# Kernel tuning notes

Hardware: AMD Instinct MI355X
Metric: run time of the kernel (lower is better)

Reference implementation:

```python
import jax, jax.numpy as jnp
import numpy as np

B, H, W, C, E, TOP_K = 16, 64, 64, 384, 5, 2


def setup_inputs() -> dict:
    key = jax.random.key(0)
    k1, k2, k3 = jax.random.split(key, 3)
    x = jax.random.normal(k1, (B, H, W, C), dtype=jnp.float32)
    Wg = jax.random.normal(k2, (C, E), dtype=jnp.float32) * 0.02   # router
    We = jax.random.normal(k3, (E, C, C), dtype=jnp.float32) * 0.02  # expert weights
    be = jnp.zeros((E, C), dtype=jnp.float32)                       # expert biases
    return {"x": x, "Wg": Wg, "We": We, "be": be}


def reference(x, Wg, We, be):
    Bx, Hx, Wx, Cx = x.shape
    Ex = Wg.shape[1]
    t = x.reshape(-1, Cx)                      # [N, C] tokens
    N = t.shape[0]

    # --- top-k routing ---
    logits = t @ Wg                            # [N, E]
    top_vals, top_idx = jax.lax.top_k(logits, TOP_K)   # [N, 2]
    gates = jax.nn.softmax(top_vals, axis=-1)          # softmax over selected experts
    combine = jnp.zeros((N, Ex), dtype=t.dtype)
    combine = combine.at[jnp.arange(N)[:, None], top_idx].set(gates)  # [N, E] sparse combine weights

    # --- expert computation (dense over experts, combined with sparse gates) ---
    expert_out = jnp.einsum('nc,ecd->ned', t, We) + be[None]  # [N, E, C]
    y = jnp.einsum('ne,ned->nd', combine, expert_out)         # [N, C]

    # --- LeakyReLU (default slope 0.01); dropout is identity in eval mode ---
    y = jax.nn.leaky_relu(y, negative_slope=0.01)
    return y.reshape(Bx, Hx, Wx, Cx)
```

## Files before the change

kernel.cpp:

```cpp
#include <hip/hip_runtime.h>
#include <stdint.h>

#define TOKENS 65536
#define CDIM 384
#define NEXP 5
#define NPAIR 10
#define CAP 8192
#define NBLK 1024
#define WE_STRIDE (CDIM * CDIM)

typedef __attribute__((ext_vector_type(8))) short short8;
typedef __attribute__((ext_vector_type(4))) float floatx4;

__constant__ int PAIR_A[NPAIR] = {0, 0, 0, 0, 1, 1, 1, 2, 2, 3};
__constant__ int PAIR_B[NPAIR] = {1, 2, 3, 4, 2, 3, 4, 3, 4, 4};

__device__ inline unsigned short f2bf(float f) {
    union { float f; uint32_t u; } v; v.f = f;
    uint32_t r = v.u + 0x7fffu + ((v.u >> 16) & 1u);
    return (unsigned short)(r >> 16);
}

__device__ inline void load_lds16(const void* g, void* l) {
    __builtin_amdgcn_global_load_lds((const __attribute__((address_space(1))) void*)g,
                                     (__attribute__((address_space(3))) void*)l, 16, 0, 0);
}

__global__ __launch_bounds__(256) void router_kernel(const float* __restrict__ x,
                                                     const float* __restrict__ Wg,
                                                     int* __restrict__ blkcnt,
                                                     int* __restrict__ tmeta,
                                                     float2* __restrict__ tgate) {
    __shared__ __align__(16) float  xs[64 * 129];
    __shared__ __align__(16) float  wgs[CDIM * 8];
    __shared__ __align__(16) double part[4 * 64 * NEXP];
    __shared__ __align__(16) double lg[64 * NEXP];
    int t = threadIdx.x, lane = t & 63, w = t >> 6;
    int tok0 = blockIdx.x * 64;

    for (int i = t; i < CDIM * NEXP; i += 256) wgs[(i / NEXP) * 8 + (i % NEXP)] = Wg[i];

    int lrow = t >> 5, loff = (t & 31) * 4;
    double p0 = 0, p1 = 0, p2 = 0, p3 = 0, p4 = 0;
    #pragma unroll
    for (int ch = 0; ch < 3; ++ch) {
        __syncthreads();
        #pragma unroll
        for (int r8 = 0; r8 < 8; ++r8) {
            int row = r8 * 8 + lrow;
            float4 v = *(const float4*)&x[(size_t)(tok0 + row) * CDIM + ch * 128 + loff];
            float* d = &xs[row * 129 + loff];
            d[0] = v.x; d[1] = v.y; d[2] = v.z; d[3] = v.w;
        }
        __syncthreads();
        const float* xr = &xs[lane * 129 + w * 32];
        #pragma unroll
        for (int j = 0; j < 32; ++j) {
            int c = ch * 128 + w * 32 + j;
            float4 w03 = *(const float4*)&wgs[c * 8];
            float  w4  = wgs[c * 8 + 4];
            double xd = (double)xr[j];
            p0 += xd * w03.x; p1 += xd * w03.y; p2 += xd * w03.z;
            p3 += xd * w03.w; p4 += xd * w4;
        }
    }
    double* pr = &part[(w * 64 + lane) * NEXP];
    pr[0] = p0; pr[1] = p1; pr[2] = p2; pr[3] = p3; pr[4] = p4;
    __syncthreads();

    for (int item = t; item < 64 * NEXP; item += 256) {
        lg[item] = part[item] + part[320 + item] + part[640 + item] + part[960 + item];
    }
    __syncthreads();

    if (t < 64) {
        double pa[NEXP];
        #pragma unroll
        for (int e = 0; e < NEXP; ++e) pa[e] = lg[t * NEXP + e];
        int i0 = 0; double m0v = pa[0];
        #pragma unroll
        for (int e = 1; e < NEXP; ++e) if (pa[e] > m0v) { m0v = pa[e]; i0 = e; }
        int i1 = -1; double m1v = -1e300;
        #pragma unroll
        for (int e = 0; e < NEXP; ++e) if (e != i0 && pa[e] > m1v) { m1v = pa[e]; i1 = e; }
        float d  = (float)(m1v - m0v);
        float e1 = expf(d);
        float inv = 1.0f / (1.0f + e1);

        int a  = i0 < i1 ? i0 : i1;
        int b2 = i0 < i1 ? i1 : i0;
        int p  = a * 4 - ((a * (a - 1)) >> 1) + (b2 - a - 1);
        float ga = (a == i0) ? inv : e1 * inv;
        float gb = (a == i0) ? e1 * inv : inv;

        unsigned long long below = (1ull << lane) - 1ull;
        int myrank = 0, myh = 0;
        #pragma unroll
        for (int e = 0; e < NPAIR; ++e) {
            unsigned long long mask = __ballot(p == e);
            if (p == e)    myrank = (int)__popcll(mask & below);
            if (lane == e) myh    = (int)__popcll(mask);
        }
        tmeta[tok0 + lane] = p | (myrank << 8);
        tgate[tok0 + lane] = make_float2(ga, gb);
        if (lane < NPAIR) blkcnt[lane * NBLK + blockIdx.x] = myh;
    }
}

__global__ __launch_bounds__(256) void mid_kernel(const int* __restrict__ blkcnt,
                                                  const int* __restrict__ tmeta,
                                                  int* __restrict__ bidx,
                                                  int* __restrict__ cnt,
                                                  const float* __restrict__ We,
                                                  unsigned short* __restrict__ WeT) {
    __shared__ float tile[64][65];
    __shared__ int   sbase[NPAIR][4];
    __shared__ int   rred[4];
    int bid = blockIdx.x;
    int t = threadIdx.x;

    if (bid >= 256) {
        int idx = bid - 256;
        int e   = idx / 36, rem = idx % 36;
        int c0  = (rem / 6) * 64, d0 = (rem % 6) * 64;
        const float* src = We + (size_t)e * WE_STRIDE;
        int dr = t & 15, cr = t >> 4;
        for (int s = 0; s < 64; s += 16) {
            float4 v = *(const float4*)&src[(size_t)(c0 + cr + s) * CDIM + d0 + dr * 4];
            tile[cr + s][dr * 4 + 0] = v.x;
            tile[cr + s][dr * 4 + 1] = v.y;
            tile[cr + s][dr * 4 + 2] = v.z;
            tile[cr + s][dr * 4 + 3] = v.w;
        }
        __syncthreads();
        unsigned short* dst = WeT + (size_t)e * WE_STRIDE;
        int c4 = t & 15, drow = t >> 4;
        for (int s = 0; s < 64; s += 16) {
            int d = drow + s;
            ushort4 o;
            o.x = f2bf(tile[c4 * 4 + 0][d]);
            o.y = f2bf(tile[c4 * 4 + 1][d]);
            o.z = f2bf(tile[c4 * 4 + 2][d]);
            o.w = f2bf(tile[c4 * 4 + 3][d]);
            *(ushort4*)&dst[(size_t)(d0 + d) * CDIM + c0 + c4 * 4] = o;
        }
        return;
    }

    int lane = t & 63, w = t >> 6;
    int nb4 = bid * 4;
    for (int p = 0; p < NPAIR; ++p) {
        int s = 0;
        for (int j = t; j < nb4; j += 256) s += blkcnt[p * NBLK + j];
        #pragma unroll
        for (int d = 1; d < 64; d <<= 1) s += __shfl_xor(s, d);
        if (lane == 0) rred[w] = s;
        __syncthreads();
        if (t == 0) {
            int S  = rred[0] + rred[1] + rred[2] + rred[3];
            int c0_ = blkcnt[p * NBLK + nb4 + 0];
            int c1_ = blkcnt[p * NBLK + nb4 + 1];
            int c2_ = blkcnt[p * NBLK + nb4 + 2];
            sbase[p][0] = S;
            sbase[p][1] = S + c0_;
            sbase[p][2] = S + c0_ + c1_;
            sbase[p][3] = S + c0_ + c1_ + c2_;
            if (bid == 255) cnt[p] = S + c0_ + c1_ + c2_ + blkcnt[p * NBLK + nb4 + 3];
        }
        __syncthreads();
    }
    int tok  = bid * 256 + t;
    int meta = tmeta[tok];
    int p    = meta & 255, rank = meta >> 8;
    int pos  = sbase[p][t >> 6] + rank;
    if (pos < CAP) bidx[p * CAP + pos] = tok;
}

__global__ __launch_bounds__(512, 4) void moe_kernel(const float* __restrict__ x,
                                                     const unsigned short* __restrict__ WeT,
                                                     const int* __restrict__ cnt,
                                                     const int* __restrict__ bidx,
                                                     const float2* __restrict__ tgate,
                                                     const float* __restrict__ be,
                                                     float* __restrict__ out) {
    int bh  = blockIdx.x;
    int bid = (bh & 7) * 240 + (bh >> 3);
    int pq  = bid / 3;
    int nt  = bid - pq * 3;
    int p   = pq >> 6;
    int mt  = pq & 63;

    int nct = cnt[p];
    int m0  = mt * 128;
    if (m0 >= nct) return;
    int valid = nct - m0; if (valid > 128) valid = 128;

    int ea = PAIR_A[p], eb = PAIR_B[p];
    int n0 = nt * 128;
    int t = threadIdx.x, lane = t & 63, wid = t >> 6;
    int wm = wid >> 1, wn = wid & 1;
    int q = lane >> 4, cc = lane & 15;

    __shared__ __align__(16) unsigned short S[4096 * 8];

    floatx4 acc[2][2][4];
    #pragma unroll
    for (int e = 0; e < 2; ++e)
        #pragma unroll
        for (int i = 0; i < 2; ++i)
            #pragma unroll
            for (int j = 0; j < 4; ++j)
                acc[e][i][j] = (floatx4){0.0f, 0.0f, 0.0f, 0.0f};

    int rrow = t >> 2, gp = t & 3;
    int gl = (gp - (rrow >> 1)) & 3;
    const unsigned short* bsrcA = WeT + (size_t)ea * WE_STRIDE + (size_t)(n0 + rrow) * CDIM + gl * 8;
    const unsigned short* bsrcB = WeT + (size_t)eb * WE_STRIDE + (size_t)(n0 + rrow) * CDIM + gl * 8;
    int bdstA = wid * 64;
    int bdstB = 512 + wid * 64;

    int srow = t >> 2, sp = t & 3;
    int arow = m0 + (srow < valid ? srow : valid - 1);
    int gi = bidx[p * CAP + arow];
    const float* xrow = x + (size_t)gi * CDIM + sp * 8;
    int agr = 4 * srow + ((sp + (srow >> 1)) & 3);

    int perm = (q + (cc >> 1)) & 3;
    int a_gr = 4 * (wm * 32 + cc) + perm;
    int b_gr = 4 * (wn * 64 + cc) + perm;

    float4 xreg[2][2];
    xreg[0][0] = *(const float4*)(xrow);
    xreg[0][1] = *(const float4*)(xrow + 4);
    xreg[1][0] = *(const float4*)(xrow + 32);
    xreg[1][1] = *(const float4*)(xrow + 36);
    load_lds16(bsrcA,      S + (size_t)(1024 + bdstA) * 8);
    load_lds16(bsrcB,      S + (size_t)(1024 + bdstB) * 8);
    load_lds16(bsrcA + 32, S + (size_t)(2048 + bdstA) * 8);
    load_lds16(bsrcB + 32, S + (size_t)(2048 + bdstB) * 8);

    #pragma unroll
    for (int kc = 0; kc < 12; ++kc) {
        int buf = kc & 1;
        int bb  = kc - (kc / 3) * 3;
        float4 a0 = xreg[buf][0], a1 = xreg[buf][1];
        short8 av;
        av[0] = f2bf(a0.x); av[1] = f2bf(a0.y); av[2] = f2bf(a0.z); av[3] = f2bf(a0.w);
        av[4] = f2bf(a1.x); av[5] = f2bf(a1.y); av[6] = f2bf(a1.z); av[7] = f2bf(a1.w);
        *(short8*)&S[(size_t)(buf * 512 + agr) * 8] = av;

        if (kc == 0 || kc == 11) {
            asm volatile("s_waitcnt vmcnt(0) lgkmcnt(0)" ::: "memory");
        } else {
            asm volatile("s_waitcnt vmcnt(4) lgkmcnt(0)" ::: "memory");
        }
        __builtin_amdgcn_s_barrier();
        __builtin_amdgcn_sched_barrier(0);

        if (kc < 10) {
            int k2 = (kc + 2) * 32;
            int nb = (kc + 2) % 3;
            xreg[buf][0] = *(const float4*)(xrow + k2);
            xreg[buf][1] = *(const float4*)(xrow + k2 + 4);
            load_lds16(bsrcA + k2, S + (size_t)(1024 + nb * 1024 + bdstA) * 8);
            load_lds16(bsrcB + k2, S + (size_t)(1024 + nb * 1024 + bdstB) * 8);
        }

        int ao = buf * 512, bo = 1024 + bb * 1024;
        short8 af0 = *(const short8*)&S[(size_t)(ao + a_gr) * 8];
        short8 af1 = *(const short8*)&S[(size_t)(ao + a_gr + 64) * 8];
        __builtin_amdgcn_s_setprio(1);
        #pragma unroll
        for (int e = 0; e < 2; ++e) {
            #pragma unroll
            for (int j = 0; j < 4; ++j) {
                short8 bf = *(const short8*)&S[(size_t)(bo + b_gr + e * 512 + j * 64) * 8];
                acc[e][0][j] = __builtin_amdgcn_mfma_f32_16x16x32_bf16(af0, bf, acc[e][0][j], 0, 0, 0);
                acc[e][1][j] = __builtin_amdgcn_mfma_f32_16x16x32_bf16(af1, bf, acc[e][1][j], 0, 0, 0);
            }
        }
        __builtin_amdgcn_s_setprio(0);
    }

    __syncthreads();
    float2* Gp = (float2*)S;
    int*    Ip = (int*)((char*)S + 1024);
    if (t < 128) {
        int rr = m0 + (t < valid ? t : valid - 1);
        int gid = bidx[p * CAP + rr];
        Ip[t] = gid;
        Gp[t] = tgate[gid];
    }
    float ba_[4], bb_[4];
    #pragma unroll
    for (int j = 0; j < 4; ++j) {
        int oc = n0 + wn * 64 + j * 16 + cc;
        ba_[j] = be[ea * CDIM + oc];
        bb_[j] = be[eb * CDIM + oc];
    }
    __syncthreads();

    #pragma unroll
    for (int i = 0; i < 2; ++i) {
        #pragma unroll
        for (int rr4 = 0; rr4 < 4; ++rr4) {
            int trow = wm * 32 + i * 16 + q * 4 + rr4;
            if (trow < valid) {
                float2 g = Gp[trow];
                int gid  = Ip[trow];
                #pragma unroll
                for (int j = 0; j < 4; ++j) {
                    int oc = n0 + wn * 64 + j * 16 + cc;
                    float v = g.x * (acc[0][i][j][rr4] + ba_[j])
                            + g.y * (acc[1][i][j][rr4] + bb_[j]);
                    v = v > 0.0f ? v : 0.01f * v;
                    out[(size_t)gid * CDIM + oc] = v;
                }
            }
        }
    }
}

extern "C" void kernel_launch(void* const* d_in, const int* in_sizes, int n_in,
                              void* d_out, int out_size, void* d_ws, size_t ws_size,
                              hipStream_t stream) {
    const float* x  = (const float*)d_in[0];
    const float* Wg = (const float*)d_in[1];
    const float* We = (const float*)d_in[2];
    const float* be = (const float*)d_in[3];
    float* out = (float*)d_out;

    char* ws = (char*)d_ws;
    int*            cnt    = (int*)ws;
    int*            bidx   = (int*)(ws + 256);
    int*            blkcnt = (int*)(ws + 327936);
    int*            tmeta  = (int*)(ws + 409856);
    float2*         tgate  = (float2*)(ws + 672000);
    unsigned short* WeT    = (unsigned short*)(ws + 1196288);

    router_kernel<<<NBLK, 256, 0, stream>>>(x, Wg, blkcnt, tmeta, tgate);
    mid_kernel<<<436, 256, 0, stream>>>(blkcnt, tmeta, bidx, cnt, We, WeT);
    moe_kernel<<<NPAIR * 64 * 3, 512, 0, stream>>>(x, WeT, cnt, bidx, tgate, be, out);
}
```

Baseline: 249.7 us.

## Shrink MoE N-tile, load A fragments directly, and simplify router reduction

The router now has four lanes per token read x straight from global memory and reduce with shuffles, replacing the LDS staging and cross-wave double reduction. A per-wave rank offset keeps the pair ordering. The MoE GEMM halves the N tile to 64 and doubles the grid. Each wave now loads and converts its own A fragments in registers, with no LDS round-trip for A. This cuts LDS to allow 6 blocks per CU, but x is re-read and re-converted by six N tiles instead of three, and by both wn waves.

Result: slower. 372.8 us (+49.3%).

```diff
diff --git a/kernel.cpp b/kernel.cpp
--- a/kernel.cpp
+++ b/kernel.cpp
@@ -31,52 +31,40 @@
                                                      int* __restrict__ blkcnt,
                                                      int* __restrict__ tmeta,
                                                      float2* __restrict__ tgate) {
-    __shared__ __align__(16) float  xs[64 * 129];
-    __shared__ __align__(16) float  wgs[CDIM * 8];
-    __shared__ __align__(16) double part[4 * 64 * NEXP];
-    __shared__ __align__(16) double lg[64 * NEXP];
+    __shared__ __align__(16) float wgs[CDIM * 8];
+    __shared__ int wcnt[4][NPAIR];
     int t = threadIdx.x, lane = t & 63, w = t >> 6;
     int tok0 = blockIdx.x * 64;
 
     for (int i = t; i < CDIM * NEXP; i += 256) wgs[(i / NEXP) * 8 + (i % NEXP)] = Wg[i];
-
-    int lrow = t >> 5, loff = (t & 31) * 4;
+    __syncthreads();
+
+    int lt = lane >> 2, g = lane & 3;
+    int token = tok0 + w * 16 + lt;
+    const float4* xb = (const float4*)(x + (size_t)token * CDIM) + g;
     double p0 = 0, p1 = 0, p2 = 0, p3 = 0, p4 = 0;
     #pragma unroll
-    for (int ch = 0; ch < 3; ++ch) {
-        __syncthreads();
-        #pragma unroll
-        for (int r8 = 0; r8 < 8; ++r8) {
-            int row = r8 * 8 + lrow;
-            float4 v = *(const float4*)&x[(size_t)(tok0 + row) * CDIM + ch * 128 + loff];
-            float* d = &xs[row * 129 + loff];
-            d[0] = v.x; d[1] = v.y; d[2] = v.z; d[3] = v.w;
-        }
-        __syncthreads();
-        const float* xr = &xs[lane * 129 + w * 32];
-        #pragma unroll
-        for (int j = 0; j < 32; ++j) {
-            int c = ch * 128 + w * 32 + j;
+    for (int k = 0; k < 24; ++k) {
+        float4 xv = xb[k * 4];
+        #pragma unroll
+        for (int u = 0; u < 4; ++u) {
+            int c = k * 16 + g * 4 + u;
+            float xe = (u == 0) ? xv.x : (u == 1) ? xv.y : (u == 2) ? xv.z : xv.w;
             float4 w03 = *(const float4*)&wgs[c * 8];
             float  w4  = wgs[c * 8 + 4];
-            double xd = (double)xr[j];
+            double xd = (double)xe;
             p0 += xd * w03.x; p1 += xd * w03.y; p2 += xd * w03.z;
             p3 += xd * w03.w; p4 += xd * w4;
         }
     }
-    double* pr = &part[(w * 64 + lane) * NEXP];
-    pr[0] = p0; pr[1] = p1; pr[2] = p2; pr[3] = p3; pr[4] = p4;
-    __syncthreads();
-
-    for (int item = t; item < 64 * NEXP; item += 256) {
-        lg[item] = part[item] + part[320 + item] + part[640 + item] + part[960 + item];
-    }
-    __syncthreads();
-
-    if (t < 64) {
-        double pa[NEXP];
-        #pragma unroll
-        for (int e = 0; e < NEXP; ++e) pa[e] = lg[t * NEXP + e];
+    p0 += __shfl_xor(p0, 1); p1 += __shfl_xor(p1, 1); p2 += __shfl_xor(p2, 1);
+    p3 += __shfl_xor(p3, 1); p4 += __shfl_xor(p4, 1);
+    p0 += __shfl_xor(p0, 2); p1 += __shfl_xor(p1, 2); p2 += __shfl_xor(p2, 2);
+    p3 += __shfl_xor(p3, 2); p4 += __shfl_xor(p4, 2);
+
+    int myp = -1; float ga = 0.0f, gb = 0.0f;
+    if (g == 0) {
+        double pa[NEXP] = {p0, p1, p2, p3, p4};
         int i0 = 0; double m0v = pa[0];
         #pragma unroll
         for (int e = 1; e < NEXP; ++e) if (pa[e] > m0v) { m0v = pa[e]; i0 = e; }
@@ -86,25 +74,31 @@
         float d  = (float)(m1v - m0v);
         float e1 = expf(d);
         float inv = 1.0f / (1.0f + e1);
-
         int a  = i0 < i1 ? i0 : i1;
         int b2 = i0 < i1 ? i1 : i0;
-        int p  = a * 4 - ((a * (a - 1)) >> 1) + (b2 - a - 1);
-        float ga = (a == i0) ? inv : e1 * inv;
-        float gb = (a == i0) ? e1 * inv : inv;
-
-        unsigned long long below = (1ull << lane) - 1ull;
-        int myrank = 0, myh = 0;
-        #pragma unroll
-        for (int e = 0; e < NPAIR; ++e) {
-            unsigned long long mask = __ballot(p == e);
-            if (p == e)    myrank = (int)__popcll(mask & below);
-            if (lane == e) myh    = (int)__popcll(mask);
-        }
-        tmeta[tok0 + lane] = p | (myrank << 8);
-        tgate[tok0 + lane] = make_float2(ga, gb);
-        if (lane < NPAIR) blkcnt[lane * NBLK + blockIdx.x] = myh;
-    }
+        myp = a * 4 - ((a * (a - 1)) >> 1) + (b2 - a - 1);
+        ga = (a == i0) ? inv : e1 * inv;
+        gb = (a == i0) ? e1 * inv : inv;
+    }
+    unsigned long long below = (1ull << lane) - 1ull;
+    int myrank = 0, myh = 0;
+    #pragma unroll
+    for (int e = 0; e < NPAIR; ++e) {
+        unsigned long long mask = __ballot(myp == e);
+        if (myp == e)  myrank = (int)__popcll(mask & below);
+        if (lane == e) myh    = (int)__popcll(mask);
+    }
+    if (lane < NPAIR) wcnt[w][lane] = myh;
+    __syncthreads();
+    if (g == 0) {
+        int woff = 0;
+        #pragma unroll
+        for (int k = 0; k < 4; ++k) if (k < w) woff += wcnt[k][myp];
+        tmeta[token] = myp | ((woff + myrank) << 8);
+        tgate[token] = make_float2(ga, gb);
+    }
+    if (t < NPAIR)
+        blkcnt[t * NBLK + blockIdx.x] = wcnt[0][t] + wcnt[1][t] + wcnt[2][t] + wcnt[3][t];
 }
 
 __global__ __launch_bounds__(256) void mid_kernel(const int* __restrict__ blkcnt,
@@ -176,7 +170,7 @@
     if (pos < CAP) bidx[p * CAP + pos] = tok;
 }
 
-__global__ __launch_bounds__(512, 4) void moe_kernel(const float* __restrict__ x,
+__global__ __launch_bounds__(512, 6) void moe_kernel(const float* __restrict__ x,
                                                      const unsigned short* __restrict__ WeT,
                                                      const int* __restrict__ cnt,
                                                      const int* __restrict__ bidx,
@@ -184,9 +178,9 @@
                                                      const float* __restrict__ be,
                                                      float* __restrict__ out) {
     int bh  = blockIdx.x;
-    int bid = (bh & 7) * 240 + (bh >> 3);
-    int pq  = bid / 3;
-    int nt  = bid - pq * 3;
+    int bid = (bh & 7) * 480 + (bh >> 3);
+    int pq  = bid / 6;
+    int nt  = bid - pq * 6;
     int p   = pq >> 6;
     int mt  = pq & 63;
 
@@ -196,85 +190,79 @@
     int valid = nct - m0; if (valid > 128) valid = 128;
 
     int ea = PAIR_A[p], eb = PAIR_B[p];
-    int n0 = nt * 128;
+    int n0 = nt * 64;
     int t = threadIdx.x, lane = t & 63, wid = t >> 6;
     int wm = wid >> 1, wn = wid & 1;
     int q = lane >> 4, cc = lane & 15;
 
-    __shared__ __align__(16) unsigned short S[4096 * 8];
-
-    floatx4 acc[2][2][4];
+    __shared__ __align__(16) unsigned short S[1536 * 8];
+
+    floatx4 acc[2][2][2];
     #pragma unroll
     for (int e = 0; e < 2; ++e)
         #pragma unroll
         for (int i = 0; i < 2; ++i)
             #pragma unroll
-            for (int j = 0; j < 4; ++j)
+            for (int j = 0; j < 2; ++j)
                 acc[e][i][j] = (floatx4){0.0f, 0.0f, 0.0f, 0.0f};
 
-    int rrow = t >> 2, gp = t & 3;
-    int gl = (gp - (rrow >> 1)) & 3;
-    const unsigned short* bsrcA = WeT + (size_t)ea * WE_STRIDE + (size_t)(n0 + rrow) * CDIM + gl * 8;
-    const unsigned short* bsrcB = WeT + (size_t)eb * WE_STRIDE + (size_t)(n0 + rrow) * CDIM + gl * 8;
-    int bdstA = wid * 64;
-    int bdstB = 512 + wid * 64;
-
-    int srow = t >> 2, sp = t & 3;
-    int arow = m0 + (srow < valid ? srow : valid - 1);
-    int gi = bidx[p * CAP + arow];
-    const float* xrow = x + (size_t)gi * CDIM + sp * 8;
-    int agr = 4 * srow + ((sp + (srow >> 1)) & 3);
+    int et = t >> 8, pe = t & 255, r = pe >> 2, gp = pe & 3;
+    int gl = (gp - (r >> 1)) & 3;
+    int esel = et ? eb : ea;
+    const unsigned short* bsrc = WeT + (size_t)esel * WE_STRIDE + (size_t)(n0 + r) * CDIM + gl * 8;
+    int bdst = wid * 64;
+
+    int r0 = wm * 32 + cc, r1 = r0 + 16;
+    int gid0 = bidx[p * CAP + m0 + (r0 < valid ? r0 : valid - 1)];
+    int gid1 = bidx[p * CAP + m0 + (r1 < valid ? r1 : valid - 1)];
+    const float* xa0 = x + (size_t)gid0 * CDIM + q * 8;
+    const float* xa1 = x + (size_t)gid1 * CDIM + q * 8;
 
     int perm = (q + (cc >> 1)) & 3;
-    int a_gr = 4 * (wm * 32 + cc) + perm;
-    int b_gr = 4 * (wn * 64 + cc) + perm;
-
-    float4 xreg[2][2];
-    xreg[0][0] = *(const float4*)(xrow);
-    xreg[0][1] = *(const float4*)(xrow + 4);
-    xreg[1][0] = *(const float4*)(xrow + 32);
-    xreg[1][1] = *(const float4*)(xrow + 36);
-    load_lds16(bsrcA,      S + (size_t)(1024 + bdstA) * 8);
-    load_lds16(bsrcB,      S + (size_t)(1024 + bdstB) * 8);
-    load_lds16(bsrcA + 32, S + (size_t)(2048 + bdstA) * 8);
-    load_lds16(bsrcB + 32, S + (size_t)(2048 + bdstB) * 8);
+    int b_gr = 4 * (wn * 32 + cc) + perm;
+
+    load_lds16(bsrc,      S + (size_t)(0 * 512 + bdst) * 8);
+    load_lds16(bsrc + 32, S + (size_t)(1 * 512 + bdst) * 8);
+    float4 xf0, xf1, xf2, xf3;
+    xf0 = *(const float4*)(xa0);
+    xf1 = *(const float4*)(xa0 + 4);
+    xf2 = *(const float4*)(xa1);
+    xf3 = *(const float4*)(xa1 + 4);
 
     #pragma unroll
     for (int kc = 0; kc < 12; ++kc) {
-        int buf = kc & 1;
-        int bb  = kc - (kc / 3) * 3;
-        float4 a0 = xreg[buf][0], a1 = xreg[buf][1];
-        short8 av;
-        av[0] = f2bf(a0.x); av[1] = f2bf(a0.y); av[2] = f2bf(a0.z); av[3] = f2bf(a0.w);
-        av[4] = f2bf(a1.x); av[5] = f2bf(a1.y); av[6] = f2bf(a1.z); av[7] = f2bf(a1.w);
-        *(short8*)&S[(size_t)(buf * 512 + agr) * 8] = av;
-
-        if (kc == 0 || kc == 11) {
-            asm volatile("s_waitcnt vmcnt(0) lgkmcnt(0)" ::: "memory");
-        } else {
-            asm volatile("s_waitcnt vmcnt(4) lgkmcnt(0)" ::: "memory");
-        }
+        int bb = kc - (kc / 3) * 3;
+        short8 af0, af1;
+        af0[0] = f2bf(xf0.x); af0[1] = f2bf(xf0.y); af0[2] = f2bf(xf0.z); af0[3] = f2bf(xf0.w);
+        af0[4] = f2bf(xf1.x); af0[5] = f2bf(xf1.y); af0[6] = f2bf(xf1.z); af0[7] = f2bf(xf1.w);
+        af1[0] = f2bf(xf2.x); af1[1] = f2bf(xf2.y); af1[2] = f2bf(xf2.z); af1[3] = f2bf(xf2.w);
+        af1[4] = f2bf(xf3.x); af1[5] = f2bf(xf3.y); af1[6] = f2bf(xf3.z); af1[7] = f2bf(xf3.w);
+
+        if (kc == 0) { asm volatile("s_waitcnt vmcnt(0)" ::: "memory"); }
+        else         { asm volatile("s_waitcnt vmcnt(1)" ::: "memory"); }
         __builtin_amdgcn_s_barrier();
         __builtin_amdgcn_sched_barrier(0);
 
+        if (kc < 11) {
+            int k1 = (kc + 1) * 32;
+            xf0 = *(const float4*)(xa0 + k1);
+            xf1 = *(const float4*)(xa0 + k1 + 4);
+            xf2 = *(const float4*)(xa1 + k1);
+            xf3 = *(const float4*)(xa1 + k1 + 4);
+        }
         if (kc < 10) {
             int k2 = (kc + 2) * 32;
             int nb = (kc + 2) % 3;
-            xreg[buf][0] = *(const float4*)(xrow + k2);
-            xreg[buf][1] = *(const float4*)(xrow + k2 + 4);
-            load_lds16(bsrcA + k2, S + (size_t)(1024 + nb * 1024 + bdstA) * 8);
-            load_lds16(bsrcB + k2, S + (size_t)(1024 + nb * 1024 + bdstB) * 8);
-        }
-
-        int ao = buf * 512, bo = 1024 + bb * 1024;
-        short8 af0 = *(const short8*)&S[(size_t)(ao + a_gr) * 8];
-        short8 af1 = *(const short8*)&S[(size_t)(ao + a_gr + 64) * 8];
+            load_lds16(bsrc + k2, S + (size_t)(nb * 512 + bdst) * 8);
+        }
+
+        int bo = bb * 512;
         __builtin_amdgcn_s_setprio(1);
         #pragma unroll
         for (int e = 0; e < 2; ++e) {
             #pragma unroll
-            for (int j = 0; j < 4; ++j) {
-                short8 bf = *(const short8*)&S[(size_t)(bo + b_gr + e * 512 + j * 64) * 8];
+            for (int j = 0; j < 2; ++j) {
+                short8 bf = *(const short8*)&S[(size_t)(bo + b_gr + e * 256 + j * 64) * 8];
                 acc[e][0][j] = __builtin_amdgcn_mfma_f32_16x16x32_bf16(af0, bf, acc[e][0][j], 0, 0, 0);
                 acc[e][1][j] = __builtin_amdgcn_mfma_f32_16x16x32_bf16(af1, bf, acc[e][1][j], 0, 0, 0);
             }
@@ -291,10 +279,10 @@
         Ip[t] = gid;
         Gp[t] = tgate[gid];
     }
-    float ba_[4], bb_[4];
-    #pragma unroll
-    for (int j = 0; j < 4; ++j) {
-        int oc = n0 + wn * 64 + j * 16 + cc;
+    float ba_[2], bb_[2];
+    #pragma unroll
+    for (int j = 0; j < 2; ++j) {
+        int oc = n0 + wn * 32 + j * 16 + cc;
         ba_[j] = be[ea * CDIM + oc];
         bb_[j] = be[eb * CDIM + oc];
     }
@@ -309,8 +297,8 @@
                 float2 g = Gp[trow];
                 int gid  = Ip[trow];
                 #pragma unroll
-                for (int j = 0; j < 4; ++j) {
-                    int oc = n0 + wn * 64 + j * 16 + cc;
+                for (int j = 0; j < 2; ++j) {
+                    int oc = n0 + wn * 32 + j * 16 + cc;
                     float v = g.x * (acc[0][i][j][rr4] + ba_[j])
                             + g.y * (acc[1][i][j][rr4] + bb_[j]);
                     v = v > 0.0f ? v : 0.01f * v;
@@ -340,5 +328,5 @@
 
     router_kernel<<<NBLK, 256, 0, stream>>>(x, Wg, blkcnt, tmeta, tgate);
     mid_kernel<<<436, 256, 0, stream>>>(blkcnt, tmeta, bidx, cnt, We, WeT);
-    moe_kernel<<<NPAIR * 64 * 3, 512, 0, stream>>>(x, WeT, cnt, bidx, tgate, be, out);
-}
+    moe_kernel<<<NPAIR * 64 * 6, 512, 0, stream>>>(x, WeT, cnt, bidx, tgate, be, out);
+}
```
